# Kernel optimization log

Measured on AMD Instinct MI355X. Metric: run time of the kernel, lower is better.

Reference implementation:

```python
import jax, jax.numpy as jnp
import numpy as np

B, C, L = 8, 256, 2048      # batch, res_channels, seq_len
E = 2 * C                    # attention / S4 width = 512
CH = 4                       # S4 channels
SQRT_HALF = 0.7071067811865476


def setup_inputs() -> dict:
    key = jax.random.key(0)
    ks = jax.random.split(key, 12)
    def n(k, s, sc):
        return jax.random.normal(k, s, dtype=jnp.float32) * sc
    return dict(
        x=jax.random.normal(ks[0], (B, C, L), dtype=jnp.float32),
        original=jax.random.normal(ks[1], (B, C, L), dtype=jnp.float32),
        sn_scale=jnp.ones((1, C, 1), jnp.float32),
        conv_w=n(ks[2], (E, C, 3), 0.05), conv_b=jnp.zeros((E,), jnp.float32),
        s4_ln_g=jnp.ones((E,), jnp.float32), s4_ln_b=jnp.zeros((E,), jnp.float32),
        s4_kernel=n(ks[3], (CH, E, L), 0.01),           # long-conv kernel per channel
        s4_D=n(ks[4], (CH, E), 1.0),                     # skip connection D
        s4_out_w=n(ks[5], (E, CH * E), 0.02), s4_out_b=jnp.zeros((E,), jnp.float32),
        attn_v_w=n(ks[6], (E, E), 0.02), attn_v_b=jnp.zeros((E,), jnp.float32),
        attn_o_w=n(ks[7], (E, E), 0.02), attn_o_b=jnp.zeros((E,), jnp.float32),
        res_w=n(ks[8], (C, C, 1), 0.05), res_b=jnp.zeros((C,), jnp.float32),
        skip_w=n(ks[9], (C, C, 1), 0.05), skip_b=jnp.zeros((C,), jnp.float32),
    )


def reference(x, original, sn_scale, conv_w, conv_b, s4_ln_g, s4_ln_b,
              s4_kernel, s4_D, s4_out_w, s4_out_b,
              attn_v_w, attn_v_b, attn_o_w, attn_o_b,
              res_w, res_b, skip_w, skip_b):
    eps = 1e-8
    # RMSNorm over channel dim (dim=1)
    rms = jnp.sqrt(jnp.sum(x * x, axis=1, keepdims=True)) / np.sqrt(x.shape[1]).astype(np.float32)
    x_n = sn_scale * x / (rms + eps)
    # h = x + original (pre-norm x), conv k=3 pad=1, GELU
    h = x + original
    h = jax.lax.conv_general_dilated(h, conv_w, (1,), [(1, 1)],
                                     dimension_numbers=('NCH', 'OIH', 'NCH'))
    h = jax.nn.gelu(h + conv_b[None, :, None], approximate=False)
    # --- S4 / GConv: LN over channels, FFT causal long conv, D-skip, GELU, out linear ---
    mu = h.mean(axis=1, keepdims=True)
    var = h.var(axis=1, keepdims=True)
    u = (h - mu) / jnp.sqrt(var + 1e-5) * s4_ln_g[None, :, None] + s4_ln_b[None, :, None]
    n2 = 2 * u.shape[-1]
    uf = jnp.fft.rfft(u, n=n2)                      # (B, E, F)
    kf = jnp.fft.rfft(s4_kernel, n=n2)              # (CH, E, F)
    y = jnp.fft.irfft(jnp.einsum('bhf,chf->bchf', uf, kf), n=n2)[..., :u.shape[-1]]
    y = y + s4_D[None, :, :, None] * u[:, None]     # (B, CH, E, L)
    y = jax.nn.gelu(y.reshape(y.shape[0], CH * E, y.shape[-1]), approximate=False)
    h_t = jnp.einsum('oc,bcl->bol', s4_out_w, y) + s4_out_b[None, :, None]  # (B, E, L)
    # --- local-window MHA with window_size=1: each position attends only to itself,
    # softmax over a single unmasked score == 1, so out = Wo @ (Wv @ x + bv) + bo exactly ---
    v = jnp.einsum('oe,bel->bol', attn_v_w, h_t) + attn_v_b[None, :, None]
    h_s = jnp.einsum('oe,bel->bol', attn_o_w, v) + attn_o_b[None, :, None]
    h2 = h_t + h_s
    out = jnp.tanh(h2[:, :C]) * jax.nn.sigmoid(h2[:, C:])
    res = jnp.einsum('oc,bcl->bol', res_w[:, :, 0], out) + res_b[None, :, None]
    skip = jnp.einsum('oc,bcl->bol', skip_w[:, :, 0], out) + skip_b[None, :, None]
    return ((x_n + res) * SQRT_HALF, skip)
```

## Files before the change

kernel.cpp:

```cpp
#include <hip/hip_runtime.h>
#include <hip/hip_bf16.h>
#include <math.h>

typedef __attribute__((ext_vector_type(8))) short short8;
typedef __attribute__((ext_vector_type(4))) float float4_t;
typedef __attribute__((ext_vector_type(2))) float cf2;
typedef unsigned short ushort_t;
typedef unsigned int uint_t;

#define NBL 16384

#define WS_CONVA   ((size_t)0)
#define WS_WV      ((size_t)786432)
#define WS_WO      ((size_t)1310720)
#define WS_W1      ((size_t)1835008)
#define WS_WCAT    ((size_t)3932160)
#define WS_A2      ((size_t)4194304)
#define WS_ACOMB   ((size_t)4718592)
#define WS_BCOMB   ((size_t)6815744)
#define WS_XN      ((size_t)6819840)
#define WS_H0PT    ((size_t)23597056)
#define WS_U       ((size_t)31993856)
#define WS_GT      ((size_t)65548288)
#define WS_UF      WS_GT
#define WS_KF      ((size_t)99102720)
#define WS_G       ((size_t)132657152)
#define WS_GATET   (WS_G + 25165824)
#define WS_UB      ((size_t)208162816)

__device__ __forceinline__ float gelu_f(float x) {
    float t = x * x;
    float a2 = x * fmaf(0.07135481627f, t, 1.59576912161f);
    return x / (1.f + __expf(-a2));
}
__device__ __forceinline__ float tanh_f(float a) {
    return 1.f - 2.f / (1.f + __expf(2.f * a));
}
__device__ __forceinline__ float sigmoid_f(float b) {
    return 1.f / (1.f + __expf(-b));
}

__device__ __forceinline__ unsigned int pack_bf2(float a, float b) {
#if __has_builtin(__builtin_amdgcn_cvt_pk_bf16_f32)
    auto v = __builtin_amdgcn_cvt_pk_bf16_f32(a, b);
    unsigned int r; __builtin_memcpy(&r, &v, 4); return r;
#else
    __hip_bfloat16 ha = __float2bfloat16(a), hb = __float2bfloat16(b);
    unsigned short ua = *(unsigned short*)&ha, ub = *(unsigned short*)&hb;
    return (unsigned int)ua | ((unsigned int)ub << 16);
#endif
}
__device__ __forceinline__ ushort_t f2bfu(float a) {
    __hip_bfloat16 h = __float2bfloat16(a);
    return *(ushort_t*)&h;
}
__device__ __forceinline__ cf2 unpack_c(unsigned int v) {
    cf2 r;
    r.x = __uint_as_float(v << 16);
    r.y = __uint_as_float(v & 0xffff0000u);
    return r;
}
__device__ __forceinline__ float bf2f(ushort_t u) {
    return __uint_as_float(((unsigned int)u) << 16);
}

__device__ __forceinline__ void cp16(const ushort_t* g, ushort_t* l) {
    __builtin_amdgcn_global_load_lds(
        (__attribute__((address_space(1))) void*)(void*)g,
        (__attribute__((address_space(3))) void*)l, 16, 0, 0);
}

__device__ __forceinline__ cf2 cswap(cf2 a) { return __builtin_shufflevector(a, a, 1, 0); }
template<int SGN>
__device__ __forceinline__ cf2 cmuli(cf2 a) {
    cf2 s = cswap(a);
    return s * cf2{(float)(-SGN), (float)SGN};
}
__device__ __forceinline__ cf2 cmul(cf2 a, cf2 b) {
    cf2 t = cswap(a) * cf2{-b.y, b.y};
    return a * cf2{b.x, b.x} + t;
}
__device__ __forceinline__ cf2 cmulc(cf2 a, float wr, float wi) {
    cf2 t = cswap(a) * cf2{-wi, wi};
    return a * cf2{wr, wr} + t;
}

__global__ __launch_bounds__(256) void wprep_kernel(
    const float* __restrict__ conv_w, const float* __restrict__ attn_v_w,
    const float* __restrict__ attn_o_w, const float* __restrict__ s4_out_w,
    const float* __restrict__ res_w, const float* __restrict__ skip_w,
    __hip_bfloat16* __restrict__ convA, __hip_bfloat16* __restrict__ WvT,
    __hip_bfloat16* __restrict__ WoBf, __hip_bfloat16* __restrict__ W1T,
    __hip_bfloat16* __restrict__ Wcat)
{
    const int N0 = 393216, N1 = 655360, N2c = 917504, N3 = 1966080, N4 = 2097152;
    for (int i = blockIdx.x * 256 + threadIdx.x; i < N4; i += gridDim.x * 256) {
        if (i < N0) {
            int m = i / 768, r = i - m * 768, dk = r >> 8, c = r & 255;
            convA[i] = __float2bfloat16(conv_w[m * 768 + c * 3 + dk]);
        } else if (i < N1) {
            int j = i - N0; int row = j >> 9, e = j & 511;
            WvT[j] = __float2bfloat16(attn_v_w[e * 512 + row]);
        } else if (i < N2c) {
            WoBf[i - N1] = __float2bfloat16(attn_o_w[i - N1]);
        } else if (i < N3) {
            int j = i - N2c; int ck = j >> 9, e = j & 511;
            W1T[j] = __float2bfloat16(s4_out_w[e * 2048 + ck]);
        } else {
            int j = i - N3; int m = j >> 8, c = j & 255;
            float v = (m < 256) ? res_w[m * 256 + c] : skip_w[(m - 256) * 256 + c];
            Wcat[j] = __float2bfloat16(v);
        }
    }
}

__global__ __launch_bounds__(256) void bias2_kernel(
    const __hip_bfloat16* __restrict__ A2, const float* __restrict__ s4_out_b,
    const float* __restrict__ attn_o_w, const float* __restrict__ attn_v_b,
    const float* __restrict__ attn_o_b, float* __restrict__ bcomb)
{
    __shared__ float red[256];
    int o = blockIdx.x, t = threadIdx.x;
    float s = 0.f;
    for (int e = t; e < 512; e += 256)
        s += __bfloat162float(A2[o * 512 + e]) * s4_out_b[e] + attn_o_w[o * 512 + e] * attn_v_b[e];
    red[t] = s; __syncthreads();
    for (int k = 128; k > 0; k >>= 1) { if (t < k) red[t] += red[t + k]; __syncthreads(); }
    if (t == 0) bcomb[o] = red[0] + attn_o_b[o];
}

__global__ __launch_bounds__(512) void prep_kernel(
    const float* __restrict__ x, const float* __restrict__ orig,
    const float* __restrict__ sn, ushort_t* __restrict__ xnb, ushort_t* __restrict__ h0pT)
{
    __shared__ float red[8][64];
    __shared__ ushort_t T[256 * 66];
    int blk = blockIdx.x, t = threadIdx.x;
    int lane = t & 63, cg = t >> 6;
    int b = blk >> 5, l0 = (blk & 31) << 6;
    size_t basein = (size_t)b * 524288 + l0 + lane;
    float ss = 0.f;
    for (int c = cg; c < 256; c += 8) {
        size_t idx = basein + (size_t)c * 2048;
        float xv = x[idx], ov = orig[idx];
        ss += xv * xv;
        T[c * 66 + lane] = f2bfu(xv + ov);
    }
    red[cg][lane] = ss;
    __syncthreads();
    float tot = 0.f;
    #pragma unroll
    for (int k = 0; k < 8; ++k) tot += red[k][lane];
    float inv = 1.0f / (sqrtf(tot) * 0.0625f + 1e-8f);
    __hip_bfloat16* xo = (__hip_bfloat16*)xnb;
    for (int c = cg; c < 256; c += 8) {
        size_t idx = basein + (size_t)c * 2048;
        xo[idx] = __float2bfloat16(sn[c] * x[idx] * inv);
    }
    int c2 = t & 255, half = t >> 8;
    size_t rowbase = (size_t)(b * 2050 + 1 + l0);
    for (int r = half; r < 64; r += 2)
        h0pT[(rowbase + r) * 256 + c2] = T[c2 * 66 + r];
    if ((blk & 31) == 0) {
        if (t < 256) h0pT[(size_t)(b * 2050) * 256 + t] = 0;
        else         h0pT[(size_t)(b * 2050 + 2049) * 256 + (t - 256)] = 0;
    }
}

__global__ __launch_bounds__(512) void ln_kernel(
    const ushort_t* __restrict__ h, ushort_t* __restrict__ ub,
    const float* __restrict__ gam, const float* __restrict__ bet)
{
    __shared__ float r1[8][64], r2[8][64];
    int blk = blockIdx.x, t = threadIdx.x;
    int lane = t & 63, og = t >> 6;
    int n = (blk << 6) + lane;
    float s1 = 0.f, s2 = 0.f;
    for (int o = og; o < 512; o += 8) { float v = bf2f(h[(size_t)o * NBL + n]); s1 += v; s2 += v * v; }
    r1[og][lane] = s1; r2[og][lane] = s2;
    __syncthreads();
    float mu = 0.f, m2 = 0.f;
    #pragma unroll
    for (int k = 0; k < 8; ++k) { mu += r1[k][lane]; m2 += r2[k][lane]; }
    mu *= (1.f / 512.f); m2 *= (1.f / 512.f);
    float rstd = rsqrtf(m2 - mu * mu + 1e-5f);
    int b = n >> 11, l = n & 2047;
    size_t sbase = (size_t)(b >> 1) * 4096 + 2 * l + (b & 1);
    for (int o = og; o < 512; o += 8) {
        size_t idx = (size_t)o * NBL + n;
        ub[(size_t)o * 16384 + sbase] = f2bfu((bf2f(h[idx]) - mu) * rstd * gam[o] + bet[o]);
    }
}

#define PERM(m) ((((m) & 3) << 2) | ((m) >> 2))

template<int SGN>
__device__ __forceinline__ void dft4p(cf2& a0, cf2& a1, cf2& a2, cf2& a3) {
    cf2 t0 = a0 + a2, t1 = a0 - a2, t2 = a1 + a3, t3 = a1 - a3;
    cf2 j3 = cmuli<SGN>(t3);
    a0 = t0 + t2; a2 = t0 - t2;
    a1 = t1 + j3; a3 = t1 - j3;
}
template<int SGN>
__device__ __forceinline__ void dft4p_half(cf2& a0, cf2& a1, cf2& a2, cf2& a3) {
    cf2 u0 = a0, u1 = a1;
    cf2 j1 = cmuli<SGN>(u1);
    a0 = u0 + u1; a2 = u0 - u1;
    a1 = u0 + j1; a3 = u0 - j1;
}
template<int SGN>
__device__ __forceinline__ void dft4p_out01(cf2 a0, cf2 a1, cf2 a2, cf2 a3, cf2& o0, cf2& o1) {
    cf2 t0 = a0 + a2, t1 = a0 - a2, t2 = a1 + a3, t3 = a1 - a3;
    o0 = t0 + t2;
    o1 = t1 + cmuli<SGN>(t3);
}

template<int SGN>
__device__ __forceinline__ void dft16_stepB(cf2* x) {
    const float sg = (float)SGN;
    const float C16[10] = {1.f, 0.92387953f, 0.70710678f, 0.38268343f, 0.f,
                           -0.38268343f, -0.70710678f, -0.92387953f, -1.f, -0.92387953f};
    const float S16[10] = {0.f, 0.38268343f, 0.70710678f, 0.92387953f, 1.f,
                           0.92387953f, 0.70710678f, 0.38268343f, 0.f, -0.38268343f};
    #pragma unroll
    for (int s = 1; s < 4; ++s)
        #pragma unroll
        for (int r = 1; r < 4; ++r) {
            int e = s * r;
            x[4 * s + r] = cmulc(x[4 * s + r], C16[e], sg * S16[e]);
        }
}
template<int SGN>
__device__ __forceinline__ void dft16p(cf2* x) {
    #pragma unroll
    for (int r = 0; r < 4; ++r) dft4p<SGN>(x[r], x[4 + r], x[8 + r], x[12 + r]);
    dft16_stepB<SGN>(x);
    #pragma unroll
    for (int s = 0; s < 4; ++s) dft4p<SGN>(x[4 * s], x[4 * s + 1], x[4 * s + 2], x[4 * s + 3]);
}
template<int SGN>
__device__ __forceinline__ void dft16_halfin(cf2* x) {
    #pragma unroll
    for (int r = 0; r < 4; ++r) dft4p_half<SGN>(x[r], x[4 + r], x[8 + r], x[12 + r]);
    dft16_stepB<SGN>(x);
    #pragma unroll
    for (int s = 0; s < 4; ++s) dft4p<SGN>(x[4 * s], x[4 * s + 1], x[4 * s + 2], x[4 * s + 3]);
}
template<int SGN>
__device__ __forceinline__ void dft16_halfout(cf2* x, cf2* y) {
    #pragma unroll
    for (int r = 0; r < 4; ++r) dft4p<SGN>(x[r], x[4 + r], x[8 + r], x[12 + r]);
    dft16_stepB<SGN>(x);
    #pragma unroll
    for (int s = 0; s < 4; ++s)
        dft4p_out01<SGN>(x[4 * s], x[4 * s + 1], x[4 * s + 2], x[4 * s + 3], y[s], y[4 + s]);
}

template<int SGN>
__device__ __forceinline__ void tw_after(cf2* x, float p, float invQ) {
    float s1, c1; __sincosf((float)SGN * 6.283185307179586f * p * invQ, &s1, &c1);
    cf2 w1 = {c1, s1}, w = w1;
    #pragma unroll
    for (int m = 1; m < 16; ++m) { x[PERM(m)] = cmul(x[PERM(m)], w); w = cmul(w, w1); }
}
template<int SGN>
__device__ __forceinline__ void tw_before(cf2* x, float p, float invQ) {
    float s1, c1; __sincosf((float)SGN * 6.283185307179586f * p * invQ, &s1, &c1);
    cf2 w1 = {c1, s1}, w = w1;
    #pragma unroll
    for (int j = 1; j < 16; ++j) { x[j] = cmul(x[j], w); w = cmul(w, w1); }
}

__global__ __launch_bounds__(256) void fft_fwd_kernel(
    const ushort_t* __restrict__ ubf, const float* __restrict__ s4k,
    uint4* __restrict__ uf, uint4* __restrict__ kf)
{
    __shared__ cf2 S[4368];
    int wg = blockIdx.x, t = threadIdx.x;
    cf2 x[16];
    if (wg < 2048) {
        int bp = wg >> 9, e = wg & 511;
        const unsigned int* p0 = (const unsigned int*)ubf + (size_t)e * 8192 + (size_t)bp * 2048;
        #pragma unroll
        for (int j = 0; j < 8; ++j) x[j] = unpack_c(p0[j * 256 + t]);
    } else {
        const float* p0 = s4k + (size_t)(wg - 2048) * 2048;
        #pragma unroll
        for (int j = 0; j < 8; ++j) x[j] = cf2{p0[j * 256 + t], 0.f};
    }
    dft16_halfin<-1>(x);
    tw_after<-1>(x, (float)t, 1.f / 4096.f);
    int tb = 17 * (t >> 4) + (t & 15);
    #pragma unroll
    for (int m = 0; m < 16; ++m) S[tb + 273 * m] = x[PERM(m)];
    __syncthreads();
    int b2 = 273 * (t >> 4) + (t & 15);
    #pragma unroll
    for (int j = 0; j < 16; ++j) x[j] = S[b2 + 17 * j];
    dft16p<-1>(x);
    tw_after<-1>(x, (float)(t & 15), 1.f / 256.f);
    #pragma unroll
    for (int m = 0; m < 16; ++m) S[b2 + 17 * m] = x[PERM(m)];
    __syncthreads();
    int b3 = 273 * (t >> 4) + 17 * (t & 15);
    #pragma unroll
    for (int j = 0; j < 16; ++j) x[j] = S[b3 + j];
    dft16p<-1>(x);
    const float sc = (wg < 2048) ? 1.f : (1.f / 4096.f);
    uint4* dst = ((wg < 2048) ? (uf + (size_t)wg * 1024) : (kf + (size_t)(wg - 2048) * 1024)) + 4 * t;
    #pragma unroll
    for (int q = 0; q < 4; ++q) {
        uint4 o;
        cf2 v0 = x[PERM(4 * q)] * sc, v1 = x[PERM(4 * q + 1)] * sc;
        cf2 v2 = x[PERM(4 * q + 2)] * sc, v3 = x[PERM(4 * q + 3)] * sc;
        o.x = pack_bf2(v0.x, v0.y);
        o.y = pack_bf2(v1.x, v1.y);
        o.z = pack_bf2(v2.x, v2.y);
        o.w = pack_bf2(v3.x, v3.y);
        dst[q] = o;
    }
}

__global__ __launch_bounds__(256) void fft_inv_kernel(
    const uint4* __restrict__ uf, const uint4* __restrict__ kf,
    unsigned int* __restrict__ g2)
{
    __shared__ cf2 S[4368];
    int wg = blockIdx.x, t = threadIdx.x;
    int bp = wg >> 11, ch = (wg >> 9) & 3, e = wg & 511;
    const uint4* zr = uf + (size_t)(bp * 512 + e) * 1024 + 4 * t;
    const uint4* kr = kf + (size_t)(ch * 512 + e) * 1024 + 4 * t;
    cf2 x[16];
    #pragma unroll
    for (int q = 0; q < 4; ++q) {
        uint4 a4 = zr[q], b4 = kr[q];
        x[4 * q + 0] = cmul(unpack_c(a4.x), unpack_c(b4.x));
        x[4 * q + 1] = cmul(unpack_c(a4.y), unpack_c(b4.y));
        x[4 * q + 2] = cmul(unpack_c(a4.z), unpack_c(b4.z));
        x[4 * q + 3] = cmul(unpack_c(a4.w), unpack_c(b4.w));
    }
    dft16p<1>(x);
    int b1 = 273 * (t >> 4) + 17 * (t & 15);
    #pragma unroll
    for (int m = 0; m < 16; ++m) S[b1 + m] = x[PERM(m)];
    __syncthreads();
    int b2 = 273 * (t >> 4) + (t & 15);
    #pragma unroll
    for (int j = 0; j < 16; ++j) x[j] = S[b2 + 17 * j];
    tw_before<1>(x, (float)(t & 15), 1.f / 256.f);
    dft16p<1>(x);
    #pragma unroll
    for (int m = 0; m < 16; ++m) S[b2 + 17 * m] = x[PERM(m)];
    __syncthreads();
    int b3 = 17 * (t >> 4) + (t & 15);
    #pragma unroll
    for (int j = 0; j < 16; ++j) x[j] = S[b3 + 273 * j];
    tw_before<1>(x, (float)t, 1.f / 4096.f);
    cf2 y[8];
    dft16_halfout<1>(x, y);
    unsigned int* go = g2 + (size_t)(ch * 512 + e) * 8192 + (size_t)bp * 2048;
    #pragma unroll
    for (int m = 0; m < 8; ++m)
        go[m * 256 + t] = pack_bf2(y[m].x, y[m].y);
}

__global__ __launch_bounds__(256) void gdt_kernel(
    const unsigned int* __restrict__ g2, const unsigned int* __restrict__ ub2,
    const float* __restrict__ s4D, ushort_t* __restrict__ gT)
{
    __shared__ unsigned int S2[64 * 65];
    int c0 = blockIdx.x * 64, r0 = blockIdx.y * 64;
    int t = threadIdx.x, lx = t & 63, ly0 = t >> 6;
    #pragma unroll
    for (int ly = ly0; ly < 64; ly += 4) {
        int r = r0 + ly, cp = c0 + lx;
        cf2 y2 = unpack_c(g2[(size_t)r * 8192 + cp]);
        cf2 u2 = unpack_c(ub2[(size_t)(r & 511) * 8192 + cp]);
        float d = s4D[r];
        float v0 = gelu_f(fmaf(d, u2.x, y2.x));
        float v1 = gelu_f(fmaf(d, u2.y, y2.y));
        S2[ly * 65 + lx] = pack_bf2(v0, v1);
    }
    __syncthreads();
    #pragma unroll
    for (int ly = ly0; ly < 64; ly += 4) {
        int oc = c0 + ly;
        unsigned int v = S2[lx * 65 + ly];
        int bp = oc >> 11, l = oc & 2047;
        size_t na = (size_t)(bp * 4096 + l) * 2048 + r0 + lx;
        gT[na] = (ushort_t)(v & 0xffff);
        gT[na + 4194304] = (ushort_t)(v >> 16);
    }
}

template<int BSRC, int EPI>
__global__ __launch_bounds__(256, 4) void gemm_kernel(
    const ushort_t* __restrict__ A, const ushort_t* __restrict__ Bm,
    ushort_t* __restrict__ Cb, float* __restrict__ Cf,
    int M, int N, int K,
    const float* __restrict__ bias, const float* __restrict__ bias2,
    const ushort_t* __restrict__ xnb, float* __restrict__ dout)
{
    __shared__ ushort_t SM[16384];
    const int t = threadIdx.x;
    const int n0 = blockIdx.x * 64, m0 = blockIdx.y * 128;
    const int w = t >> 6, lane = t & 63, quad = lane >> 4, lr = lane & 15;
    const int wm = (w >> 1) * 64, wn = (w & 1) * 32;

    const int srow = lane >> 2;
    const int swslot = ((lane & 3) ^ ((lane >> 3) & 3)) * 8;
    const int r0q = w * 32 + srow;
    int ar0 = m0 + r0q, ar1 = m0 + r0q + 16;
    if (EPI == 5) {
        ar0 = (r0q < 64) ? (64 * blockIdx.y + r0q) : (192 + 64 * blockIdx.y + r0q);
        int r1 = r0q + 16;
        ar1 = (r1 < 64) ? (64 * blockIdx.y + r1) : (192 + 64 * blockIdx.y + r1);
    }
    const ushort_t* aSrc0 = A + (size_t)ar0 * K + swslot;
    const ushort_t* aSrc1 = A + (size_t)ar1 * K + swslot;
    const int nrow = n0 + w * 16 + srow;
    const ushort_t* bSrc;
    if (BSRC == 0) bSrc = Bm + (size_t)nrow * K + swslot;
    else           bSrc = Bm + (size_t)((nrow >> 11) * 2050 + (nrow & 2047)) * 256 + swslot;

    const int aD = w * 1024;
    const int bD = 4096 + w * 512;

    float4_t acc[4][2];
    #pragma unroll
    for (int i = 0; i < 4; ++i)
        #pragma unroll
        for (int j = 0; j < 2; ++j) { float4_t z = {0.f, 0.f, 0.f, 0.f}; acc[i][j] = z; }

    const int qsw = (quad ^ ((lr >> 1) & 3)) << 3;

#define STAGE(BUF, KK) do {                                                     \
        cp16(aSrc0 + (KK), SM + (BUF) + aD);                                    \
        cp16(aSrc1 + (KK), SM + (BUF) + aD + 512);                              \
        if (BSRC == 0) cp16(bSrc + (KK), SM + (BUF) + bD);                      \
        else cp16(bSrc + (((KK) >> 8) * 256 + ((KK) & 255)), SM + (BUF) + bD);  \
    } while (0)

#define COMPUTE(BUF) do {                                                       \
        const ushort_t* Al = SM + (BUF);                                        \
        const ushort_t* Bl = SM + (BUF) + 4096;                                 \
        short8 af[4], bfr[2];                                                   \
        _Pragma("unroll")                                                       \
        for (int im = 0; im < 4; ++im)                                          \
            af[im] = *(const short8*)&Al[(wm + im * 16 + lr) * 32 + qsw];       \
        _Pragma("unroll")                                                       \
        for (int in_ = 0; in_ < 2; ++in_)                                       \
            bfr[in_] = *(const short8*)&Bl[(wn + in_ * 16 + lr) * 32 + qsw];    \
        _Pragma("unroll")                                                       \
        for (int im = 0; im < 4; ++im)                                          \
            _Pragma("unroll")                                                   \
            for (int in_ = 0; in_ < 2; ++in_)                                   \
                acc[im][in_] = __builtin_amdgcn_mfma_f32_16x16x32_bf16(         \
                    af[im], bfr[in_], acc[im][in_], 0, 0, 0);                   \
    } while (0)

    STAGE(0, 0);
    __syncthreads();

    for (int kt = 0; kt < K; kt += 64) {
        STAGE(8192, kt + 32);
        COMPUTE(0);
        __syncthreads();
        if (kt + 64 < K) STAGE(0, kt + 64);
        COMPUTE(8192);
        __syncthreads();
    }
#undef STAGE
#undef COMPUTE

    if (EPI == 5) {
        const int by = blockIdx.y;
        #pragma unroll
        for (int im = 0; im < 4; ++im)
            #pragma unroll
            for (int in_ = 0; in_ < 2; ++in_) {
                int nl = wn + in_ * 16 + lr;
                #pragma unroll
                for (int r = 0; r < 4; ++r) {
                    int i = wm + im * 16 + quad * 4 + r;
                    int me = (i < 64) ? (64 * by + i) : (192 + 64 * by + i);
                    SM[i * 68 + nl] = f2bfu(acc[im][in_][r] + bias[me]);
                }
            }
        __syncthreads();
        int nl = t >> 2, gcb = (t & 3) * 16;
        size_t obase = (size_t)(n0 + nl) * 256 + 64 * by + gcb;
        short8 o0, o1;
        #pragma unroll
        for (int j = 0; j < 16; ++j) {
            int gc = gcb + j;
            float a = bf2f(SM[gc * 68 + nl]);
            float bb = bf2f(SM[(gc + 64) * 68 + nl]);
            ushort_t gv = f2bfu(tanh_f(a) * sigmoid_f(bb));
            if (j < 8) o0[j] = (short)gv; else o1[j - 8] = (short)gv;
        }
        *(short8*)(Cb + obase) = o0;
        *(short8*)(Cb + obase + 8) = o1;
        return;
    }

    #pragma unroll
    for (int im = 0; im < 4; ++im) {
        #pragma unroll
        for (int in_ = 0; in_ < 2; ++in_) {
            int n = n0 + wn + in_ * 16 + lr;
            int mb = m0 + wm + im * 16 + quad * 4;
            #pragma unroll
            for (int r = 0; r < 4; ++r) {
                int m = mb + r;
                float v = acc[im][in_][r];
                if (EPI == 0) {
                    v += bias[m];
                    ((__hip_bfloat16*)Cb)[(size_t)m * N + n] = __float2bfloat16(gelu_f(v));
                } else if (EPI == 1) {
                    v += (m == n) ? 1.0f : 0.0f;
                    ((__hip_bfloat16*)Cb)[(size_t)m * N + n] = __float2bfloat16(v);
                } else if (EPI == 2) {
                    ((__hip_bfloat16*)Cb)[(size_t)m * N + n] = __float2bfloat16(v);
                } else {
                    int bb = n >> 11, ll = n & 2047;
                    if (m < 256) {
                        v += bias[m];
                        int idx = (bb << 19) + (m << 11) + ll;
                        dout[idx] = (bf2f(xnb[idx]) + v) * 0.70710678118654752f;
                    } else {
                        v += bias2[m - 256];
                        dout[4194304 + (bb << 19) + ((m - 256) << 11) + ll] = v;
                    }
                }
            }
        }
    }
}

extern "C" void kernel_launch(void* const* d_in, const int* in_sizes, int n_in,
                              void* d_out, int out_size, void* d_ws, size_t ws_size,
                              hipStream_t stream)
{
    const float* x         = (const float*)d_in[0];
    const float* original  = (const float*)d_in[1];
    const float* sn_scale  = (const float*)d_in[2];
    const float* conv_w    = (const float*)d_in[3];
    const float* conv_b    = (const float*)d_in[4];
    const float* s4_ln_g   = (const float*)d_in[5];
    const float* s4_ln_b   = (const float*)d_in[6];
    const float* s4_kernel = (const float*)d_in[7];
    const float* s4_D      = (const float*)d_in[8];
    const float* s4_out_w  = (const float*)d_in[9];
    const float* s4_out_b  = (const float*)d_in[10];
    const float* attn_v_w  = (const float*)d_in[11];
    const float* attn_v_b  = (const float*)d_in[12];
    const float* attn_o_w  = (const float*)d_in[13];
    const float* attn_o_b  = (const float*)d_in[14];
    const float* res_w     = (const float*)d_in[15];
    const float* res_b     = (const float*)d_in[16];
    const float* skip_w    = (const float*)d_in[17];
    const float* skip_b    = (const float*)d_in[18];

    char* ws = (char*)d_ws;
    __hip_bfloat16* convA = (__hip_bfloat16*)(ws + WS_CONVA);
    __hip_bfloat16* WvT   = (__hip_bfloat16*)(ws + WS_WV);
    __hip_bfloat16* WoBf  = (__hip_bfloat16*)(ws + WS_WO);
    __hip_bfloat16* W1T   = (__hip_bfloat16*)(ws + WS_W1);
    __hip_bfloat16* Wcat  = (__hip_bfloat16*)(ws + WS_WCAT);
    ushort_t* A2    = (ushort_t*)(ws + WS_A2);
    ushort_t* Acomb = (ushort_t*)(ws + WS_ACOMB);
    float* bcombp  = (float*)(ws + WS_BCOMB);
    ushort_t* xnb  = (ushort_t*)(ws + WS_XN);
    ushort_t* h0pT = (ushort_t*)(ws + WS_H0PT);
    ushort_t* hP   = (ushort_t*)(ws + WS_U);
    ushort_t* ubP  = (ushort_t*)(ws + WS_UB);
    uint4* ufP = (uint4*)(ws + WS_UF);
    uint4* kfP = (uint4*)(ws + WS_KF);
    unsigned int* g2P = (unsigned int*)(ws + WS_G);
    ushort_t* gT    = (ushort_t*)(ws + WS_GT);
    ushort_t* gateT = (ushort_t*)(ws + WS_GATET);

    wprep_kernel<<<dim3(4096), dim3(256), 0, stream>>>(conv_w, attn_v_w, attn_o_w, s4_out_w,
        res_w, skip_w, convA, WvT, WoBf, W1T, Wcat);
    gemm_kernel<0, 1><<<dim3(8, 4), dim3(256), 0, stream>>>(
        (const ushort_t*)WoBf, (const ushort_t*)WvT, A2, nullptr, 512, 512, 512,
        nullptr, nullptr, nullptr, nullptr);
    bias2_kernel<<<dim3(512), dim3(256), 0, stream>>>(
        (const __hip_bfloat16*)A2, s4_out_b, attn_o_w, attn_v_b, attn_o_b, bcombp);
    gemm_kernel<0, 2><<<dim3(32, 4), dim3(256), 0, stream>>>(
        A2, (const ushort_t*)W1T, Acomb, nullptr, 512, 2048, 512,
        nullptr, nullptr, nullptr, nullptr);

    prep_kernel<<<dim3(256), dim3(512), 0, stream>>>(x, original, sn_scale, xnb, h0pT);
    gemm_kernel<1, 0><<<dim3(256, 4), dim3(256), 0, stream>>>(
        (const ushort_t*)convA, h0pT, hP, nullptr, 512, NBL, 768,
        conv_b, nullptr, nullptr, nullptr);
    ln_kernel<<<dim3(256), dim3(512), 0, stream>>>(hP, ubP, s4_ln_g, s4_ln_b);
    fft_fwd_kernel<<<dim3(4096), dim3(256), 0, stream>>>(ubP, s4_kernel, ufP, kfP);
    fft_inv_kernel<<<dim3(8192), dim3(256), 0, stream>>>(ufP, kfP, g2P);
    gdt_kernel<<<dim3(128, 32), dim3(256), 0, stream>>>(
        g2P, (const unsigned int*)ubP, s4_D, gT);
    gemm_kernel<0, 5><<<dim3(256, 4), dim3(256), 0, stream>>>(
        (const ushort_t*)Acomb, gT, gateT, nullptr, 512, NBL, 2048,
        bcombp, nullptr, nullptr, nullptr);
    gemm_kernel<0, 4><<<dim3(256, 4), dim3(256), 0, stream>>>(
        (const ushort_t*)Wcat, gateT, nullptr, nullptr, 512, NBL, 256,
        res_b, skip_b, xnb, (float*)d_out);
}
```

Measured before the change: 406.5 us.

## Use 128x128-tile GEMM kernel with register prefetch for gated S4 output GEMM

Adds a new GEMM kernel with 128x128 output tiles (4x4 MFMA tiles per wave) and register-staged prefetch of the next K-slice into padded LDS, and uses it for the large K=2048 gated-output GEMM. The larger tile halves the number of B-operand reloads per output and raises MFMA work per LDS load, aiming to cut memory traffic on the largest GEMM. The tanh-sigmoid epilogue is now done in two passes through shared memory. In exchange it uses more accumulator registers, drops the occupancy hint, and runs with single-buffered LDS and a sync per 32-wide K step.

```diff
diff --git a/kernel.cpp b/kernel.cpp
--- a/kernel.cpp
+++ b/kernel.cpp
@@ -394,6 +394,148 @@
 }
 
 template<int BSRC, int EPI>
+__global__ __launch_bounds__(256) void gemmA_kernel(
+    const ushort_t* __restrict__ A, const ushort_t* __restrict__ Bm,
+    ushort_t* __restrict__ Cb, float* __restrict__ Cf,
+    int M, int N, int K,
+    const float* __restrict__ bias, const float* __restrict__ bias2,
+    const ushort_t* __restrict__ xnb, float* __restrict__ dout)
+{
+    __shared__ ushort_t SM[10240];
+    ushort_t* Alds = SM;
+    ushort_t* Blds = SM + 5120;
+    const int t = threadIdx.x;
+    const int n0 = blockIdx.x * 128, m0 = blockIdx.y * 128;
+    const int w = t >> 6, lane = t & 63, quad = lane >> 4, lr = lane & 15;
+    const int wm = (w >> 1) * 64, wn = (w & 1) * 64;
+
+    const int i_s = t >> 1, j0 = (t & 1) * 16;
+    int a_row = m0 + i_s;
+    if (EPI == 5) a_row = (i_s < 64) ? (64 * blockIdx.y + i_s) : (192 + 64 * blockIdx.y + i_s);
+    int bI = 0, lI = 0;
+    if (BSRC == 1) { int n = n0 + i_s; bI = n >> 11; lI = n & 2047; }
+
+    float4_t acc[4][4];
+    #pragma unroll
+    for (int i = 0; i < 4; ++i)
+        #pragma unroll
+        for (int j = 0; j < 4; ++j) { float4_t z = {0.f, 0.f, 0.f, 0.f}; acc[i][j] = z; }
+
+    short8 pa0, pa1, pb0, pb1;
+    {
+        const short8* sa = (const short8*)(A + (size_t)a_row * K + j0);
+        pa0 = sa[0]; pa1 = sa[1];
+        const ushort_t* sp;
+        if (BSRC == 0) sp = Bm + (size_t)(n0 + i_s) * K + j0;
+        else           sp = Bm + (size_t)(bI * 2050 + lI) * 256 + j0;
+        const short8* sb = (const short8*)sp;
+        pb0 = sb[0]; pb1 = sb[1];
+    }
+
+    for (int kt = 0; kt < K; kt += 32) {
+        if (kt) __syncthreads();
+        *(short8*)&Alds[i_s * 40 + j0]     = pa0;
+        *(short8*)&Alds[i_s * 40 + j0 + 8] = pa1;
+        *(short8*)&Blds[i_s * 40 + j0]     = pb0;
+        *(short8*)&Blds[i_s * 40 + j0 + 8] = pb1;
+        __syncthreads();
+        int kn = kt + 32;
+        if (kn < K) {
+            const short8* sa = (const short8*)(A + (size_t)a_row * K + kn + j0);
+            pa0 = sa[0]; pa1 = sa[1];
+            const ushort_t* sp;
+            if (BSRC == 0) sp = Bm + (size_t)(n0 + i_s) * K + kn + j0;
+            else { int dk = kn >> 8, cb = kn & 255; sp = Bm + (size_t)(bI * 2050 + lI + dk) * 256 + cb + j0; }
+            const short8* sb = (const short8*)sp;
+            pb0 = sb[0]; pb1 = sb[1];
+        }
+        short8 af[4], bfr[4];
+        #pragma unroll
+        for (int im = 0; im < 4; ++im)
+            af[im] = *(const short8*)&Alds[(wm + im * 16 + lr) * 40 + quad * 8];
+        #pragma unroll
+        for (int in_ = 0; in_ < 4; ++in_)
+            bfr[in_] = *(const short8*)&Blds[(wn + in_ * 16 + lr) * 40 + quad * 8];
+        #pragma unroll
+        for (int im = 0; im < 4; ++im)
+            #pragma unroll
+            for (int in_ = 0; in_ < 4; ++in_)
+                acc[im][in_] = __builtin_amdgcn_mfma_f32_16x16x32_bf16(af[im], bfr[in_], acc[im][in_], 0, 0, 0);
+    }
+
+    if (EPI == 5) {
+        const int by = blockIdx.y;
+        __syncthreads();
+        #pragma unroll
+        for (int p = 0; p < 2; ++p) {
+            if (p) __syncthreads();
+            if ((w & 1) == p) {
+                #pragma unroll
+                for (int im = 0; im < 4; ++im)
+                    #pragma unroll
+                    for (int in_ = 0; in_ < 4; ++in_) {
+                        int nl = in_ * 16 + lr;
+                        #pragma unroll
+                        for (int r = 0; r < 4; ++r) {
+                            int i = wm + im * 16 + quad * 4 + r;
+                            int me = (i < 64) ? (64 * by + i) : (192 + 64 * by + i);
+                            SM[i * 68 + nl] = f2bfu(acc[im][in_][r] + bias[me]);
+                        }
+                    }
+            }
+            __syncthreads();
+            int nl = t >> 2, gcb = (t & 3) * 16;
+            size_t obase = (size_t)(n0 + 64 * p + nl) * 256 + 64 * by + gcb;
+            short8 o0, o1;
+            #pragma unroll
+            for (int j = 0; j < 16; ++j) {
+                int gc = gcb + j;
+                float a = bf2f(SM[gc * 68 + nl]);
+                float bb = bf2f(SM[(gc + 64) * 68 + nl]);
+                ushort_t gv = f2bfu(tanh_f(a) * sigmoid_f(bb));
+                if (j < 8) o0[j] = (short)gv; else o1[j - 8] = (short)gv;
+            }
+            *(short8*)(Cb + obase) = o0;
+            *(short8*)(Cb + obase + 8) = o1;
+        }
+        return;
+    }
+
+    #pragma unroll
+    for (int im = 0; im < 4; ++im) {
+        #pragma unroll
+        for (int in_ = 0; in_ < 4; ++in_) {
+            int n = n0 + wn + in_ * 16 + lr;
+            int mb = m0 + wm + im * 16 + quad * 4;
+            #pragma unroll
+            for (int r = 0; r < 4; ++r) {
+                int m = mb + r;
+                float v = acc[im][in_][r];
+                if (EPI == 0) {
+                    v += bias[m];
+                    ((__hip_bfloat16*)Cb)[(size_t)m * N + n] = __float2bfloat16(gelu_f(v));
+                } else if (EPI == 1) {
+                    v += (m == n) ? 1.0f : 0.0f;
+                    ((__hip_bfloat16*)Cb)[(size_t)m * N + n] = __float2bfloat16(v);
+                } else if (EPI == 2) {
+                    ((__hip_bfloat16*)Cb)[(size_t)m * N + n] = __float2bfloat16(v);
+                } else {
+                    int bb = n >> 11, ll = n & 2047;
+                    if (m < 256) {
+                        v += bias[m];
+                        int idx = (bb << 19) + (m << 11) + ll;
+                        dout[idx] = (bf2f(xnb[idx]) + v) * 0.70710678118654752f;
+                    } else {
+                        v += bias2[m - 256];
+                        dout[4194304 + (bb << 19) + ((m - 256) << 11) + ll] = v;
+                    }
+                }
+            }
+        }
+    }
+}
+
+template<int BSRC, int EPI>
 __global__ __launch_bounds__(256, 4) void gemm_kernel(
     const ushort_t* __restrict__ A, const ushort_t* __restrict__ Bm,
     ushort_t* __restrict__ Cb, float* __restrict__ Cf,
@@ -411,11 +553,6 @@
     const int swslot = ((lane & 3) ^ ((lane >> 3) & 3)) * 8;
     const int r0q = w * 32 + srow;
     int ar0 = m0 + r0q, ar1 = m0 + r0q + 16;
-    if (EPI == 5) {
-        ar0 = (r0q < 64) ? (64 * blockIdx.y + r0q) : (192 + 64 * blockIdx.y + r0q);
-        int r1 = r0q + 16;
-        ar1 = (r1 < 64) ? (64 * blockIdx.y + r1) : (192 + 64 * blockIdx.y + r1);
-    }
     const ushort_t* aSrc0 = A + (size_t)ar0 * K + swslot;
     const ushort_t* aSrc1 = A + (size_t)ar1 * K + swslot;
     const int nrow = n0 + w * 16 + srow;
@@ -472,37 +609,6 @@
     }
 #undef STAGE
 #undef COMPUTE
-
-    if (EPI == 5) {
-        const int by = blockIdx.y;
-        #pragma unroll
-        for (int im = 0; im < 4; ++im)
-            #pragma unroll
-            for (int in_ = 0; in_ < 2; ++in_) {
-                int nl = wn + in_ * 16 + lr;
-                #pragma unroll
-                for (int r = 0; r < 4; ++r) {
-                    int i = wm + im * 16 + quad * 4 + r;
-                    int me = (i < 64) ? (64 * by + i) : (192 + 64 * by + i);
-                    SM[i * 68 + nl] = f2bfu(acc[im][in_][r] + bias[me]);
-                }
-            }
-        __syncthreads();
-        int nl = t >> 2, gcb = (t & 3) * 16;
-        size_t obase = (size_t)(n0 + nl) * 256 + 64 * by + gcb;
-        short8 o0, o1;
-        #pragma unroll
-        for (int j = 0; j < 16; ++j) {
-            int gc = gcb + j;
-            float a = bf2f(SM[gc * 68 + nl]);
-            float bb = bf2f(SM[(gc + 64) * 68 + nl]);
-            ushort_t gv = f2bfu(tanh_f(a) * sigmoid_f(bb));
-            if (j < 8) o0[j] = (short)gv; else o1[j - 8] = (short)gv;
-        }
-        *(short8*)(Cb + obase) = o0;
-        *(short8*)(Cb + obase + 8) = o1;
-        return;
-    }
 
     #pragma unroll
     for (int im = 0; im < 4; ++im) {
@@ -601,7 +707,7 @@
     fft_inv_kernel<<<dim3(8192), dim3(256), 0, stream>>>(ufP, kfP, g2P);
     gdt_kernel<<<dim3(128, 32), dim3(256), 0, stream>>>(
         g2P, (const unsigned int*)ubP, s4_D, gT);
-    gemm_kernel<0, 5><<<dim3(256, 4), dim3(256), 0, stream>>>(
+    gemmA_kernel<0, 5><<<dim3(128, 4), dim3(256), 0, stream>>>(
         (const ushort_t*)Acomb, gT, gateT, nullptr, 512, NBL, 2048,
         bcombp, nullptr, nullptr, nullptr);
     gemm_kernel<0, 4><<<dim3(256, 4), dim3(256), 0, stream>>>(
```

Result: slower. 424.7 us (+4.5%).

## Pre-swizzle GEMM operands into MFMA fragment layout and use LDS-free gate GEMM

Applied to the files above, without the earlier changes.

The gdt kernel and the Acomb-producing GEMM now write their outputs directly in a per-lane MFMA fragment order. A new gemmF kernel can then load A and B fragments straight from global memory into registers with double buffering, skipping LDS staging and barriers in the main loop. It uses 128-wide N tiles with 4x4 accumulators per wave. This removes shared-memory traffic and syncs from the largest GEMM, but it relies on cache reuse instead of LDS and needs more registers.

```diff
diff --git a/kernel.cpp b/kernel.cpp
--- a/kernel.cpp
+++ b/kernel.cpp
@@ -382,14 +382,94 @@
         S2[ly * 65 + lx] = pack_bf2(v0, v1);
     }
     __syncthreads();
+    int rr = r0 + lx;
+    size_t rpart = (size_t)(rr >> 5) * 524288 + (size_t)(((rr >> 3) & 3) * 128 + (rr & 7));
     #pragma unroll
     for (int ly = ly0; ly < 64; ly += 4) {
         int oc = c0 + ly;
         unsigned int v = S2[lx * 65 + ly];
         int bp = oc >> 11, l = oc & 2047;
-        size_t na = (size_t)(bp * 4096 + l) * 2048 + r0 + lx;
-        gT[na] = (ushort_t)(v & 0xffff);
-        gT[na + 4194304] = (ushort_t)(v >> 16);
+        int n_lo = bp * 4096 + l;
+        size_t npart = (size_t)(n_lo >> 6) * 2048 + (size_t)(((n_lo >> 4) & 3) * 512 + (n_lo & 15) * 8);
+        gT[rpart + npart]         = (ushort_t)(v & 0xffff);
+        gT[rpart + npart + 65536] = (ushort_t)(v >> 16);
+    }
+}
+
+__global__ __launch_bounds__(256) void gemmF_kernel(
+    const ushort_t* __restrict__ Af, const ushort_t* __restrict__ Bf,
+    ushort_t* __restrict__ Cb, const float* __restrict__ bias)
+{
+    __shared__ ushort_t SM[8704];
+    const int t = threadIdx.x;
+    const int w = t >> 6, lane = t & 63, quad = lane >> 4, lr = lane & 15;
+    const int wm = (w >> 1) * 64;
+    const int by = blockIdx.y, n0 = blockIdx.x * 128;
+    const int h = (w >> 1) ? (4 + by) : by;
+    const int nb = (n0 >> 6) + (w & 1);
+
+    const ushort_t* Aw = Af + (size_t)h * 2048 + (size_t)lane * 8;
+    const ushort_t* Bw = Bf + (size_t)nb * 2048 + (size_t)lane * 8;
+
+    float4_t acc[4][4];
+    #pragma unroll
+    for (int i = 0; i < 4; ++i)
+        #pragma unroll
+        for (int j = 0; j < 4; ++j) { float4_t z = {0.f, 0.f, 0.f, 0.f}; acc[i][j] = z; }
+
+    short8 a0[4], a1[4], b0[4], b1[4];
+
+#define LDA(D, S) do { _Pragma("unroll") for (int i_ = 0; i_ < 4; ++i_) \
+        D[i_] = *(const short8*)(Aw + (size_t)(S) * 16384 + i_ * 512); } while (0)
+#define LDB(D, S) do { _Pragma("unroll") for (int i_ = 0; i_ < 4; ++i_) \
+        D[i_] = *(const short8*)(Bw + (size_t)(S) * 524288 + i_ * 512); } while (0)
+#define CMP(AA, BB) do { _Pragma("unroll") for (int im_ = 0; im_ < 4; ++im_) \
+        _Pragma("unroll") for (int in_ = 0; in_ < 4; ++in_) \
+            acc[im_][in_] = __builtin_amdgcn_mfma_f32_16x16x32_bf16(AA[im_], BB[in_], acc[im_][in_], 0, 0, 0); } while (0)
+
+    LDA(a0, 0); LDB(b0, 0);
+    LDA(a1, 1); LDB(b1, 1);
+    for (int s = 0; s < 64; s += 2) {
+        CMP(a0, b0);
+        if (s + 2 < 64) { LDA(a0, s + 2); LDB(b0, s + 2); }
+        CMP(a1, b1);
+        if (s + 3 < 64) { LDA(a1, s + 3); LDB(b1, s + 3); }
+    }
+#undef LDA
+#undef LDB
+#undef CMP
+
+    #pragma unroll
+    for (int p = 0; p < 2; ++p) {
+        if (p) __syncthreads();
+        if ((w & 1) == p) {
+            #pragma unroll
+            for (int im = 0; im < 4; ++im)
+                #pragma unroll
+                for (int in_ = 0; in_ < 4; ++in_) {
+                    int nl = in_ * 16 + lr;
+                    #pragma unroll
+                    for (int r = 0; r < 4; ++r) {
+                        int i = wm + im * 16 + quad * 4 + r;
+                        int me = (i < 64) ? (64 * by + i) : (192 + 64 * by + i);
+                        SM[i * 68 + nl] = f2bfu(acc[im][in_][r] + bias[me]);
+                    }
+                }
+        }
+        __syncthreads();
+        int nl = t >> 2, gcb = (t & 3) * 16;
+        size_t obase = (size_t)(n0 + 64 * p + nl) * 256 + 64 * by + gcb;
+        short8 o0, o1;
+        #pragma unroll
+        for (int j = 0; j < 16; ++j) {
+            int gc = gcb + j;
+            float a = bf2f(SM[gc * 68 + nl]);
+            float bb = bf2f(SM[(gc + 64) * 68 + nl]);
+            ushort_t gv = f2bfu(tanh_f(a) * sigmoid_f(bb));
+            if (j < 8) o0[j] = (short)gv; else o1[j - 8] = (short)gv;
+        }
+        *(short8*)(Cb + obase) = o0;
+        *(short8*)(Cb + obase + 8) = o1;
     }
 }
 
@@ -411,11 +491,6 @@
     const int swslot = ((lane & 3) ^ ((lane >> 3) & 3)) * 8;
     const int r0q = w * 32 + srow;
     int ar0 = m0 + r0q, ar1 = m0 + r0q + 16;
-    if (EPI == 5) {
-        ar0 = (r0q < 64) ? (64 * blockIdx.y + r0q) : (192 + 64 * blockIdx.y + r0q);
-        int r1 = r0q + 16;
-        ar1 = (r1 < 64) ? (64 * blockIdx.y + r1) : (192 + 64 * blockIdx.y + r1);
-    }
     const ushort_t* aSrc0 = A + (size_t)ar0 * K + swslot;
     const ushort_t* aSrc1 = A + (size_t)ar1 * K + swslot;
     const int nrow = n0 + w * 16 + srow;
@@ -473,37 +548,6 @@
 #undef STAGE
 #undef COMPUTE
 
-    if (EPI == 5) {
-        const int by = blockIdx.y;
-        #pragma unroll
-        for (int im = 0; im < 4; ++im)
-            #pragma unroll
-            for (int in_ = 0; in_ < 2; ++in_) {
-                int nl = wn + in_ * 16 + lr;
-                #pragma unroll
-                for (int r = 0; r < 4; ++r) {
-                    int i = wm + im * 16 + quad * 4 + r;
-                    int me = (i < 64) ? (64 * by + i) : (192 + 64 * by + i);
-                    SM[i * 68 + nl] = f2bfu(acc[im][in_][r] + bias[me]);
-                }
-            }
-        __syncthreads();
-        int nl = t >> 2, gcb = (t & 3) * 16;
-        size_t obase = (size_t)(n0 + nl) * 256 + 64 * by + gcb;
-        short8 o0, o1;
-        #pragma unroll
-        for (int j = 0; j < 16; ++j) {
-            int gc = gcb + j;
-            float a = bf2f(SM[gc * 68 + nl]);
-            float bb = bf2f(SM[(gc + 64) * 68 + nl]);
-            ushort_t gv = f2bfu(tanh_f(a) * sigmoid_f(bb));
-            if (j < 8) o0[j] = (short)gv; else o1[j - 8] = (short)gv;
-        }
-        *(short8*)(Cb + obase) = o0;
-        *(short8*)(Cb + obase + 8) = o1;
-        return;
-    }
-
     #pragma unroll
     for (int im = 0; im < 4; ++im) {
         #pragma unroll
@@ -521,7 +565,9 @@
                     v += (m == n) ? 1.0f : 0.0f;
                     ((__hip_bfloat16*)Cb)[(size_t)m * N + n] = __float2bfloat16(v);
                 } else if (EPI == 2) {
-                    ((__hip_bfloat16*)Cb)[(size_t)m * N + n] = __float2bfloat16(v);
+                    size_t fi = ((((size_t)(n >> 5) * 8 + (m >> 6)) * 4 + ((m >> 4) & 3)) * 64
+                                 + ((n >> 3) & 3) * 16 + (m & 15)) * 8 + (n & 7);
+                    Cb[fi] = f2bfu(v);
                 } else {
                     int bb = n >> 11, ll = n & 2047;
                     if (m < 256) {
@@ -601,9 +647,8 @@
     fft_inv_kernel<<<dim3(8192), dim3(256), 0, stream>>>(ufP, kfP, g2P);
     gdt_kernel<<<dim3(128, 32), dim3(256), 0, stream>>>(
         g2P, (const unsigned int*)ubP, s4_D, gT);
-    gemm_kernel<0, 5><<<dim3(256, 4), dim3(256), 0, stream>>>(
-        (const ushort_t*)Acomb, gT, gateT, nullptr, 512, NBL, 2048,
-        bcombp, nullptr, nullptr, nullptr);
+    gemmF_kernel<<<dim3(128, 4), dim3(256), 0, stream>>>(
+        (const ushort_t*)Acomb, gT, gateT, bcombp);
     gemm_kernel<0, 4><<<dim3(256, 4), dim3(256), 0, stream>>>(
         (const ushort_t*)Wcat, gateT, nullptr, nullptr, 512, NBL, 256,
         res_b, skip_b, xnb, (float*)d_out);
```

New measurement: 423.5 us. 4.2% more time.
